# Optimization experiments

Measured on AMD Instinct MI355X. Metric: run time of the kernel, lower is better.

The kernel has to match this reference:

```python
import jax, jax.numpy as jnp
import numpy as np

# Real spherical harmonics, l=2 (2l+1 = 5 components), standard normalization.
C_XY   = float(0.5  * np.sqrt(15.0 / np.pi))
C_Z2   = float(0.25 * np.sqrt(5.0  / np.pi))
C_X2Y2 = float(0.25 * np.sqrt(15.0 / np.pi))

N_NODES  = 50000
N_EDGES  = 1_600_000
HIDDEN   = 32
CHANNELS = 16


def _sph_harm_l2(u):
    # u: [E,3] unit vectors -> [E,5]
    x, y, z = u[..., 0], u[..., 1], u[..., 2]
    return jnp.stack([
        C_XY * x * y,
        C_XY * y * z,
        C_Z2 * (3.0 * z * z - 1.0),
        C_XY * x * z,
        C_X2Y2 * (x * x - y * y),
    ], axis=-1)


def setup_inputs() -> dict:
    key = jax.random.key(0)
    k = jax.random.split(key, 6)
    positions = jax.random.normal(k[0], (N_NODES, 3), dtype=jnp.float32) * 10.0
    edge_index = jax.random.randint(k[1], (2, N_EDGES), 0, N_NODES)
    # radial MLP: dist [E,1] -> relu -> [E,CHANNELS]
    W1 = jax.random.normal(k[2], (1, HIDDEN), dtype=jnp.float32)
    b1 = jax.random.normal(k[3], (HIDDEN,), dtype=jnp.float32) * 0.1
    W2 = jax.random.normal(k[4], (HIDDEN, CHANNELS), dtype=jnp.float32) / np.sqrt(HIDDEN)
    b2 = jax.random.normal(k[5], (CHANNELS,), dtype=jnp.float32) * 0.1
    return {"positions": positions, "W1": W1, "b1": b1, "W2": W2, "b2": b2,
            "edge_index": edge_index}


def reference(positions, W1, b1, W2, b2, edge_index):
    i_arr = edge_index[0]
    j_arr = edge_index[1]
    # per-edge relative vectors + distances (point_cloud.getVectors / getDistance)
    rel = positions[i_arr] - positions[j_arr]            # [E,3]
    dist = jnp.linalg.norm(rel, axis=-1, keepdims=True)  # [E,1]
    dist = jnp.maximum(dist, 1e-8)                       # guard degenerate edges
    unit = rel / dist                                    # normalized vectors
    sh = _sph_harm_l2(unit)                              # [E,5] spharm(l_filter)
    # calculateRadialValues: radial MLP on distances -> [E,CHANNELS]
    h = jax.nn.relu(dist @ W1 + b1)
    radial = h @ W2 + b2
    # filter = spherical harmonics broadcast * per-channel radial values
    return radial[:, :, None] * sh[:, None, :]           # [E,CHANNELS,5]
```

## Files before the change

kernel.cpp:

```cpp
#include <hip/hip_runtime.h>
#include <math.h>

#define E_CNT 1600000
#define HID 32
#define CH 16
#define NSEG 33
#define AB (NSEG * CH)
#define TILE 256
#define RSTR 17
#define SSTR 6

#define C_XY   1.0925484305920792f
#define C_Z2   0.31539156525252005f
#define C_X2Y2 0.5462742152960396f

__global__ void precompute_kernel(const float* __restrict__ W1,
                                  const float* __restrict__ b1,
                                  const float* __restrict__ W2,
                                  const float* __restrict__ b2,
                                  float* __restrict__ ws) {
    __shared__ float s_v[HID], s_w1[HID], s_b1[HID];
    __shared__ int s_rank[HID];
    int tid = threadIdx.x;
    if (tid < HID) {
        float w = W1[tid], b = b1[tid];
        float v = 0.0f;
        if (w != 0.0f) v = fmaxf(-b / w, 0.0f);
        s_v[tid] = v; s_w1[tid] = w; s_b1[tid] = b;
    }
    __syncthreads();
    if (tid < HID) {
        float v = s_v[tid];
        int r = 0;
        for (int k = 0; k < HID; ++k) {
            float vk = s_v[k];
            r += (vk < v || (vk == v && k < tid)) ? 1 : 0;
        }
        s_rank[tid] = r;
        ws[tid] = v;
    }
    __syncthreads();
    if (tid < AB) {
        int m = tid / CH;
        int c = tid % CH;
        float A = 0.0f, B = b2[c];
        for (int k = 0; k < HID; ++k) {
            float w = s_w1[k], b = s_b1[k];
            bool act;
            if (w > 0.0f)      act = (s_rank[k] < m);
            else if (w < 0.0f) act = (s_rank[k] >= m);
            else               act = (b > 0.0f);
            if (act) {
                float w2 = W2[k * CH + c];
                A = fmaf(w, w2, A);
                B = fmaf(b, w2, B);
            }
        }
        ws[HID + tid]      = A;
        ws[HID + AB + tid] = B;
    }
}

__global__ __launch_bounds__(256) void edge_kernel(const float* __restrict__ pos,
                                                   const int* __restrict__ ei,
                                                   const float* __restrict__ ws,
                                                   float* __restrict__ out) {
    __shared__ __align__(16) float sA[AB];
    __shared__ __align__(16) float sB[AB];
    __shared__ float sR[TILE * RSTR];
    __shared__ float sSH[TILE * SSTR];

    const int t = threadIdx.x;
    for (int q = t; q < AB; q += 256) {
        sA[q] = ws[HID + q];
        sB[q] = ws[HID + AB + q];
    }
    float vbp[HID];
#pragma unroll
    for (int k = 0; k < HID; ++k) vbp[k] = ws[k];
    __syncthreads();

    const int e = blockIdx.x * TILE + t;
    {
        int i = ei[e];
        int j = ei[E_CNT + e];
        const float* pi = pos + 3 * i;
        const float* pj = pos + 3 * j;
        float rx = pi[0] - pj[0];
        float ry = pi[1] - pj[1];
        float rz = pi[2] - pj[2];
        float d2 = fmaf(rx, rx, fmaf(ry, ry, rz * rz));
        float dist = fmaxf(sqrtf(d2), 1e-8f);
        float inv = __builtin_amdgcn_rcpf(dist);
        float x = rx * inv, y = ry * inv, z = rz * inv;
        sSH[t * SSTR + 0] = C_XY * x * y;
        sSH[t * SSTR + 1] = C_XY * y * z;
        sSH[t * SSTR + 2] = C_Z2 * fmaf(3.0f * z, z, -1.0f);
        sSH[t * SSTR + 3] = C_XY * x * z;
        sSH[t * SSTR + 4] = C_X2Y2 * (x * x - y * y);

        int m = 0;
#pragma unroll
        for (int k = 0; k < HID; ++k) m += (vbp[k] < dist) ? 1 : 0;

        const float4* Ar = reinterpret_cast<const float4*>(&sA[m * CH]);
        const float4* Br = reinterpret_cast<const float4*>(&sB[m * CH]);
#pragma unroll
        for (int q = 0; q < 4; ++q) {
            float4 a = Ar[q], b = Br[q];
            sR[t * RSTR + 4 * q + 0] = fmaf(dist, a.x, b.x);
            sR[t * RSTR + 4 * q + 1] = fmaf(dist, a.y, b.y);
            sR[t * RSTR + 4 * q + 2] = fmaf(dist, a.z, b.z);
            sR[t * RSTR + 4 * q + 3] = fmaf(dist, a.w, b.w);
        }
    }
    __syncthreads();

    float4* ob = reinterpret_cast<float4*>(out) + (size_t)blockIdx.x * (TILE * 20);
#pragma unroll
    for (int it = 0; it < 20; ++it) {
        int idx4 = t + 256 * it;
        int el = idx4 / 20;
        int p  = (idx4 - el * 20) * 4;
        const float* rr = &sR[el * RSTR];
        const float* ss = &sSH[el * SSTR];
        float4 o;
        o.x = rr[(p + 0) / 5] * ss[(p + 0) % 5];
        o.y = rr[(p + 1) / 5] * ss[(p + 1) % 5];
        o.z = rr[(p + 2) / 5] * ss[(p + 2) % 5];
        o.w = rr[(p + 3) / 5] * ss[(p + 3) % 5];
        ob[idx4] = o;
    }
}

extern "C" void kernel_launch(void* const* d_in, const int* in_sizes, int n_in,
                              void* d_out, int out_size, void* d_ws, size_t ws_size,
                              hipStream_t stream) {
    const float* pos = (const float*)d_in[0];
    const float* W1  = (const float*)d_in[1];
    const float* b1  = (const float*)d_in[2];
    const float* W2  = (const float*)d_in[3];
    const float* b2  = (const float*)d_in[4];
    const int*   ei  = (const int*)d_in[5];
    float* out = (float*)d_out;
    float* ws  = (float*)d_ws;

    precompute_kernel<<<1, 544, 0, stream>>>(W1, b1, W2, b2, ws);
    edge_kernel<<<E_CNT / TILE, TILE, 0, stream>>>(pos, ei, ws, out);
}
```

Before: 119.5 us.

## Fuse radial-table precompute into edge kernel and hoist output index math

Removes the separate single-block precompute launch and rebuilds the piecewise-linear radial MLP table redundantly inside every edge block, overlapping it with the position gathers. The tile grows to 320 edges so each thread's output slot pattern (t%20) stays fixed across iterations, which lets the divide/modulo index math be hoisted out of the store loop. The table layout is changed to a channel-quad-major interleave. In exchange, every block repeats the table computation (about 528 entries × 32 steps) and does an extra barrier, which could cost more than the launch it saves.

```diff
diff --git a/kernel.cpp b/kernel.cpp
--- a/kernel.cpp
+++ b/kernel.cpp
@@ -5,131 +5,139 @@
 #define HID 32
 #define CH 16
 #define NSEG 33
-#define AB (NSEG * CH)
-#define TILE 256
+#define TILE 320
+#define GRID (E_CNT / TILE)
 #define RSTR 17
-#define SSTR 6
+#define SSTR 7
 
 #define C_XY   1.0925484305920792f
 #define C_Z2   0.31539156525252005f
 #define C_X2Y2 0.5462742152960396f
 
-__global__ void precompute_kernel(const float* __restrict__ W1,
-                                  const float* __restrict__ b1,
-                                  const float* __restrict__ W2,
-                                  const float* __restrict__ b2,
-                                  float* __restrict__ ws) {
-    __shared__ float s_v[HID], s_w1[HID], s_b1[HID];
-    __shared__ int s_rank[HID];
-    int tid = threadIdx.x;
-    if (tid < HID) {
-        float w = W1[tid], b = b1[tid];
+__global__ __launch_bounds__(TILE) void edge_kernel(
+    const float* __restrict__ pos,
+    const int*   __restrict__ ei,
+    const float* __restrict__ W1,
+    const float* __restrict__ b1,
+    const float* __restrict__ W2,
+    const float* __restrict__ b2,
+    float* __restrict__ out)
+{
+    __shared__ float s_v[HID];
+    __shared__ int   s_rank[HID];
+    __shared__ __align__(16) float sTab[8 * NSEG * 4];
+    __shared__ float sR[TILE * RSTR];
+    __shared__ float sSH[TILE * SSTR];
+
+    const int t = threadIdx.x;
+    const int e = blockIdx.x * TILE + t;
+
+    const int ni = ei[e];
+    const int nj = ei[E_CNT + e];
+
+    float vbp[HID];
+#pragma unroll
+    for (int k = 0; k < HID; ++k) {
+        float w = W1[k], b = b1[k];
         float v = 0.0f;
         if (w != 0.0f) v = fmaxf(-b / w, 0.0f);
-        s_v[tid] = v; s_w1[tid] = w; s_b1[tid] = b;
+        vbp[k] = __int_as_float(__builtin_amdgcn_readfirstlane(__float_as_int(v)));
+    }
+
+    const float* pi = pos + 3 * ni;
+    const float* pj = pos + 3 * nj;
+    const float rx = pi[0] - pj[0];
+    const float ry = pi[1] - pj[1];
+    const float rz = pi[2] - pj[2];
+
+    if (t == 0) {
+#pragma unroll
+        for (int k = 0; k < HID; ++k) s_v[k] = vbp[k];
     }
     __syncthreads();
-    if (tid < HID) {
-        float v = s_v[tid];
+
+    if (t < HID) {
+        const float mv = s_v[t];
         int r = 0;
+#pragma unroll
+        for (int k = 0; k < HID; ++k)
+            r += (vbp[k] < mv || (vbp[k] == mv && k < t)) ? 1 : 0;
+        s_rank[t] = r;
+    }
+
+    const float d2   = fmaf(rx, rx, fmaf(ry, ry, rz * rz));
+    const float dist = fmaxf(sqrtf(d2), 1e-8f);
+    const float inv  = __builtin_amdgcn_rcpf(dist);
+    const float x = rx * inv, y = ry * inv, z = rz * inv;
+    sSH[t * SSTR + 0] = C_XY * x * y;
+    sSH[t * SSTR + 1] = C_XY * y * z;
+    sSH[t * SSTR + 2] = C_Z2 * fmaf(3.0f * z, z, -1.0f);
+    sSH[t * SSTR + 3] = C_XY * x * z;
+    sSH[t * SSTR + 4] = C_X2Y2 * (x * x - y * y);
+
+    int m = 0;
+#pragma unroll
+    for (int k = 0; k < HID; ++k) m += (vbp[k] < dist) ? 1 : 0;
+
+    __syncthreads();
+
+    for (int idx = t; idx < NSEG * CH; idx += TILE) {
+        const int sm = idx / CH;
+        const int c  = idx % CH;
+        float A = 0.0f, B = b2[c];
+#pragma unroll
         for (int k = 0; k < HID; ++k) {
-            float vk = s_v[k];
-            r += (vk < v || (vk == v && k < tid)) ? 1 : 0;
-        }
-        s_rank[tid] = r;
-        ws[tid] = v;
-    }
-    __syncthreads();
-    if (tid < AB) {
-        int m = tid / CH;
-        int c = tid % CH;
-        float A = 0.0f, B = b2[c];
-        for (int k = 0; k < HID; ++k) {
-            float w = s_w1[k], b = s_b1[k];
+            const float w = W1[k], b = b1[k];
             bool act;
-            if (w > 0.0f)      act = (s_rank[k] < m);
-            else if (w < 0.0f) act = (s_rank[k] >= m);
+            if (w > 0.0f)      act = (s_rank[k] < sm);
+            else if (w < 0.0f) act = (s_rank[k] >= sm);
             else               act = (b > 0.0f);
             if (act) {
-                float w2 = W2[k * CH + c];
+                const float w2 = W2[k * CH + c];
                 A = fmaf(w, w2, A);
                 B = fmaf(b, w2, B);
             }
         }
-        ws[HID + tid]      = A;
-        ws[HID + AB + tid] = B;
+        const int q = c >> 2, xc = c & 3;
+        sTab[(q * NSEG + sm) * 4 + xc]       = A;
+        sTab[((q + 4) * NSEG + sm) * 4 + xc] = B;
     }
-}
-
-__global__ __launch_bounds__(256) void edge_kernel(const float* __restrict__ pos,
-                                                   const int* __restrict__ ei,
-                                                   const float* __restrict__ ws,
-                                                   float* __restrict__ out) {
-    __shared__ __align__(16) float sA[AB];
-    __shared__ __align__(16) float sB[AB];
-    __shared__ float sR[TILE * RSTR];
-    __shared__ float sSH[TILE * SSTR];
-
-    const int t = threadIdx.x;
-    for (int q = t; q < AB; q += 256) {
-        sA[q] = ws[HID + q];
-        sB[q] = ws[HID + AB + q];
-    }
-    float vbp[HID];
-#pragma unroll
-    for (int k = 0; k < HID; ++k) vbp[k] = ws[k];
     __syncthreads();
 
-    const int e = blockIdx.x * TILE + t;
     {
-        int i = ei[e];
-        int j = ei[E_CNT + e];
-        const float* pi = pos + 3 * i;
-        const float* pj = pos + 3 * j;
-        float rx = pi[0] - pj[0];
-        float ry = pi[1] - pj[1];
-        float rz = pi[2] - pj[2];
-        float d2 = fmaf(rx, rx, fmaf(ry, ry, rz * rz));
-        float dist = fmaxf(sqrtf(d2), 1e-8f);
-        float inv = __builtin_amdgcn_rcpf(dist);
-        float x = rx * inv, y = ry * inv, z = rz * inv;
-        sSH[t * SSTR + 0] = C_XY * x * y;
-        sSH[t * SSTR + 1] = C_XY * y * z;
-        sSH[t * SSTR + 2] = C_Z2 * fmaf(3.0f * z, z, -1.0f);
-        sSH[t * SSTR + 3] = C_XY * x * z;
-        sSH[t * SSTR + 4] = C_X2Y2 * (x * x - y * y);
-
-        int m = 0;
-#pragma unroll
-        for (int k = 0; k < HID; ++k) m += (vbp[k] < dist) ? 1 : 0;
-
-        const float4* Ar = reinterpret_cast<const float4*>(&sA[m * CH]);
-        const float4* Br = reinterpret_cast<const float4*>(&sB[m * CH]);
+        const float4* T4 = reinterpret_cast<const float4*>(sTab);
 #pragma unroll
         for (int q = 0; q < 4; ++q) {
-            float4 a = Ar[q], b = Br[q];
-            sR[t * RSTR + 4 * q + 0] = fmaf(dist, a.x, b.x);
-            sR[t * RSTR + 4 * q + 1] = fmaf(dist, a.y, b.y);
-            sR[t * RSTR + 4 * q + 2] = fmaf(dist, a.z, b.z);
-            sR[t * RSTR + 4 * q + 3] = fmaf(dist, a.w, b.w);
+            const float4 a  = T4[q * NSEG + m];
+            const float4 bb = T4[(q + 4) * NSEG + m];
+            sR[t * RSTR + 4 * q + 0] = fmaf(dist, a.x, bb.x);
+            sR[t * RSTR + 4 * q + 1] = fmaf(dist, a.y, bb.y);
+            sR[t * RSTR + 4 * q + 2] = fmaf(dist, a.z, bb.z);
+            sR[t * RSTR + 4 * q + 3] = fmaf(dist, a.w, bb.w);
         }
     }
     __syncthreads();
 
-    float4* ob = reinterpret_cast<float4*>(out) + (size_t)blockIdx.x * (TILE * 20);
+    const int w20 = t % 20;
+    const int e0  = t / 20;
+    const int p   = 4 * w20;
+    const int ri0 =  p      / 5, si0 =  p      - 5 * ri0;
+    const int ri1 = (p + 1) / 5, si1 = (p + 1) - 5 * ri1;
+    const int ri2 = (p + 2) / 5, si2 = (p + 2) - 5 * ri2;
+    const int ri3 = (p + 3) / 5, si3 = (p + 3) - 5 * ri3;
+    const float* rb = &sR[e0 * RSTR];
+    const float* sb = &sSH[e0 * SSTR];
+    float4* ob = reinterpret_cast<float4*>(out) + (size_t)blockIdx.x * (TILE * 20) + t;
 #pragma unroll
     for (int it = 0; it < 20; ++it) {
-        int idx4 = t + 256 * it;
-        int el = idx4 / 20;
-        int p  = (idx4 - el * 20) * 4;
-        const float* rr = &sR[el * RSTR];
-        const float* ss = &sSH[el * SSTR];
+        const int ro = it * 16 * RSTR;
+        const int so = it * 16 * SSTR;
         float4 o;
-        o.x = rr[(p + 0) / 5] * ss[(p + 0) % 5];
-        o.y = rr[(p + 1) / 5] * ss[(p + 1) % 5];
-        o.z = rr[(p + 2) / 5] * ss[(p + 2) % 5];
-        o.w = rr[(p + 3) / 5] * ss[(p + 3) % 5];
-        ob[idx4] = o;
+        o.x = rb[ro + ri0] * sb[so + si0];
+        o.y = rb[ro + ri1] * sb[so + si1];
+        o.z = rb[ro + ri2] * sb[so + si2];
+        o.w = rb[ro + ri3] * sb[so + si3];
+        ob[it * TILE] = o;
     }
 }
 
@@ -143,8 +151,7 @@
     const float* b2  = (const float*)d_in[4];
     const int*   ei  = (const int*)d_in[5];
     float* out = (float*)d_out;
-    float* ws  = (float*)d_ws;
+    (void)ws_size; (void)d_ws; (void)in_sizes; (void)n_in; (void)out_size;
 
-    precompute_kernel<<<1, 544, 0, stream>>>(W1, b1, W2, b2, ws);
-    edge_kernel<<<E_CNT / TILE, TILE, 0, stream>>>(pos, ei, ws, out);
+    edge_kernel<<<GRID, TILE, 0, stream>>>(pos, ei, W1, b1, W2, b2, out);
 }
```

Result: slower. 153.4 us (+28.4%).
